# Kernel tuning notes

Measured on AMD Instinct MI355X. Metric: run time of the kernel, lower is better.

The kernel has to match this reference:

```python
import jax, jax.numpy as jnp
import numpy as np
import math

B, N, F = 16, 1024, 1024
OUT = 1024

def setup_inputs() -> dict:
    key = jax.random.key(0)
    k1, k2, k3, k4 = jax.random.split(key, 4)
    prott5_emd = jax.random.normal(k1, (B, N, F), dtype=jnp.float32)
    # shared (dense) normalized adjacency, as the original applies one adj to every sample
    adj = jax.random.uniform(k2, (N, N), dtype=jnp.float32)
    adj = adj / jnp.sum(adj, axis=1, keepdims=True)  # row-normalize like a GCN propagation matrix
    h0 = jax.random.normal(k3, (B, N, F), dtype=jnp.float32)
    stdv = 1.0 / math.sqrt(OUT)
    weight = jax.random.uniform(k4, (F, OUT), minval=-stdv, maxval=stdv, dtype=jnp.float32)
    return {"prott5_emd": prott5_emd, "adj": adj, "h0": h0, "weight": weight,
            "lamda": 0.5, "alpha": 0.1, "l": 1}

def reference(prott5_emd, adj, h0, weight, lamda, alpha, l):
    # GraphConvolution (GCNII-style), variant=False, residual=False
    theta = min(1.0, math.log(lamda / l + 1.0))  # static python scalar
    # batched aggregation: adj @ x_i for every sample i  ->  [B, N, F]
    hi = jnp.einsum('nm,bmf->bnf', adj, prott5_emd)
    support = (1.0 - alpha) * hi + alpha * h0          # affine combine with initial features
    out = theta * jnp.einsum('bnf,fo->bno', support, weight) + (1.0 - theta) * support
    return out
```

## Files before the change

### kernel.cpp

```cpp
#include <hip/hip_runtime.h>
#include <hip/hip_bf16.h>

typedef __attribute__((ext_vector_type(8))) short bf16x8;
typedef __attribute__((ext_vector_type(4))) float f32x4;
typedef __attribute__((ext_vector_type(4))) unsigned int u32x4;
typedef __attribute__((ext_vector_type(2))) unsigned int u32x2;

__device__ __forceinline__ float b2f(unsigned short u) {
  unsigned int x = ((unsigned int)u) << 16;
  float f;
  __builtin_memcpy(&f, &x, 4);
  return f;
}
__device__ __forceinline__ unsigned short f2b(float f) {
  __hip_bfloat16 h = __float2bfloat16(f);
  unsigned short u;
  __builtin_memcpy(&u, &h, 2);
  return u;
}

__global__ __launch_bounds__(256) void conv_transpose64(
    const float* __restrict__ src, unsigned short* __restrict__ dst,
    int R, int C) {
  __shared__ unsigned short tile[64][68];
  const int b = blockIdx.z;
  const float* s = src + (size_t)b * R * C;
  unsigned short* d = dst + (size_t)b * R * C;
  const int r0 = blockIdx.y * 64, c0 = blockIdx.x * 64;
  const int t = threadIdx.x;
#pragma unroll
  for (int p = 0; p < 4; ++p) {
    const int id = t + 256 * p;
    const int r = id >> 4, c4 = (id & 15) * 4;
    f32x4 v = *(const f32x4*)(s + (size_t)(r0 + r) * C + (c0 + c4));
#pragma unroll
    for (int j = 0; j < 4; ++j) tile[r][c4 + j] = f2b(v[j]);
  }
  __syncthreads();
#pragma unroll
  for (int p = 0; p < 2; ++p) {
    const int id = t + 256 * p;
    const int oc = id >> 3, cr8 = (id & 7) * 8;
    u32x4 v;
    unsigned short* pv = (unsigned short*)&v;
#pragma unroll
    for (int j = 0; j < 8; ++j) pv[j] = tile[cr8 + j][oc];
    *(u32x4*)(d + (size_t)(c0 + oc) * R + (r0 + cr8)) = v;
  }
}

__global__ __launch_bounds__(256) void conv_transpose_wprime(
    const float* __restrict__ src, unsigned short* __restrict__ dst,
    float scale, float diag) {
  __shared__ float tile[64][65];
  const int r0 = blockIdx.y * 64, c0 = blockIdx.x * 64;
  const int t = threadIdx.x;
#pragma unroll
  for (int p = 0; p < 4; ++p) {
    const int id = t + 256 * p;
    const int r = id >> 4, c4 = (id & 15) * 4;
    f32x4 v = *(const f32x4*)(src + (size_t)(r0 + r) * 1024 + (c0 + c4));
#pragma unroll
    for (int j = 0; j < 4; ++j) tile[r][c4 + j] = v[j];
  }
  __syncthreads();
#pragma unroll
  for (int p = 0; p < 2; ++p) {
    const int id = t + 256 * p;
    const int oc = id >> 3, cr8 = (id & 7) * 8;
    u32x4 v;
    unsigned short* pv = (unsigned short*)&v;
#pragma unroll
    for (int j = 0; j < 8; ++j) {
      const int o = c0 + oc, f = r0 + cr8 + j;
      float val = scale * tile[cr8 + j][oc] + (o == f ? diag : 0.f);
      pv[j] = f2b(val);
    }
    *(u32x4*)(dst + (size_t)(c0 + oc) * 1024 + (r0 + cr8)) = v;
  }
}

__global__ __launch_bounds__(256) void conv_bf16(const float* __restrict__ src,
                                                 unsigned short* __restrict__ dst,
                                                 int n) {
  const int i = (blockIdx.x * 256 + threadIdx.x) * 4;
  if (i >= n) return;
  f32x4 v = *(const f32x4*)(src + i);
  unsigned short o[4];
#pragma unroll
  for (int j = 0; j < 4; ++j) o[j] = f2b(v[j]);
  u32x2 pk;
  __builtin_memcpy(&pk, o, 8);
  *(u32x2*)(dst + i) = pk;
}

__global__ __launch_bounds__(256) void fuse_h0(
    const unsigned short* __restrict__ Sp, const float* __restrict__ Hp,
    unsigned short* __restrict__ So) {
  const size_t i = ((size_t)blockIdx.x * 256 + threadIdx.x) * 8;
  const u32x4 sv = *(const u32x4*)(Sp + i);
  const f32x4 ha = *(const f32x4*)(Hp + i);
  const f32x4 hb = *(const f32x4*)(Hp + i + 4);
  u32x4 ov;
#pragma unroll
  for (int w = 0; w < 4; ++w) {
    const float hlo = (w < 2) ? ha[2 * w] : hb[2 * w - 4];
    const float hhi = (w < 2) ? ha[2 * w + 1] : hb[2 * w - 3];
    const float r0 = b2f((unsigned short)(sv[w] & 0xffffu)) + 0.1f * hlo;
    const float r1 = b2f((unsigned short)(sv[w] >> 16)) + 0.1f * hhi;
    ov[w] = (unsigned int)f2b(r0) | ((unsigned int)f2b(r1) << 16);
  }
  *(u32x4*)(So + i) = ov;
}

__device__ __forceinline__ void stage_tile16(unsigned short* ldsbase,
                                             const unsigned short* __restrict__ gbase,
                                             size_t rowbase, int half, int k0,
                                             int t, int wv) {
#pragma unroll
  for (int l = 0; l < 2; ++l) {
    const int id = l * 512 + t;
    const int rl = id >> 3, c = id & 7;
    const int gc = (c ^ (rl & 7)) << 3;
    const unsigned short* g = gbase + (rowbase + half * 128 + rl) * 1024 + k0 + gc;
    unsigned short* dst = ldsbase + half * 8192 + (l * 512 + wv * 64) * 8;
    __builtin_amdgcn_global_load_lds(
        (const __attribute__((address_space(1))) unsigned int*)g,
        (__attribute__((address_space(3))) unsigned int*)dst, 16, 0, 0);
  }
}

#define LOAD_A(MH)                                                     \
  {                                                                    \
    const unsigned short* Ard = lds[rd * 2 + 0];                       \
    _Pragma("unroll") for (int mi = 0; mi < 4; ++mi)                   \
        _Pragma("unroll") for (int kk = 0; kk < 2; ++kk) {             \
      const int row = wm + (MH)*64 + mi * 16 + (lane & 15);            \
      const int ch = ((kk * 4 + (lane >> 4)) ^ (row & 7)) << 3;        \
      areg[mi][kk] = *(const bf16x8*)(Ard + row * 64 + ch);            \
    }                                                                  \
  }
#define LOAD_B(NH, BR)                                                 \
  {                                                                    \
    const unsigned short* Brd = lds[rd * 2 + 1];                       \
    _Pragma("unroll") for (int nj = 0; nj < 2; ++nj)                   \
        _Pragma("unroll") for (int kk = 0; kk < 2; ++kk) {             \
      const int row = wn + (NH)*32 + nj * 16 + (lane & 15);            \
      const int ch = ((kk * 4 + (lane >> 4)) ^ (row & 7)) << 3;        \
      BR[nj][kk] = *(const bf16x8*)(Brd + row * 64 + ch);              \
    }                                                                  \
  }
#define MFMA_Q(MH, NH, BR)                                             \
  do {                                                                 \
    __builtin_amdgcn_s_setprio(1);                                     \
    _Pragma("unroll") for (int mi = 0; mi < 4; ++mi)                   \
        _Pragma("unroll") for (int nj = 0; nj < 2; ++nj)               \
            _Pragma("unroll") for (int kk = 0; kk < 2; ++kk)           \
        acc[(MH)*4 + mi][(NH)*2 + nj] =                                \
        __builtin_amdgcn_mfma_f32_16x16x32_bf16(                       \
            areg[mi][kk], BR[nj][kk], acc[(MH)*4 + mi][(NH)*2 + nj],   \
            0, 0, 0);                                                  \
    __builtin_amdgcn_s_setprio(0);                                     \
  } while (0)
#define LGKM0                                          \
  asm volatile("s_waitcnt lgkmcnt(0)" ::: "memory");   \
  __builtin_amdgcn_sched_barrier(0)
#define BAR __builtin_amdgcn_s_barrier()

__global__ __launch_bounds__(512, 2) void gemm1(
    const unsigned short* __restrict__ A, const unsigned short* __restrict__ BT,
    unsigned short* __restrict__ Cq, float c0) {
  constexpr int NT = 16;
  constexpr size_t NF = 1024ull * 1024ull;
  __shared__ unsigned short lds[4][16384];
  const int bid = blockIdx.x;
  const int nid = (bid & 7) * 32 + (bid >> 3);
  const size_t m0 = (size_t)(nid >> 6) * 256, n0 = (size_t)(nid & 63) * 256;
  const int t = threadIdx.x, lane = t & 63, wv = t >> 6;
  const int wm = (wv >> 2) * 128, wn = (wv & 3) * 64;

  f32x4 acc[8][4];
#pragma unroll
  for (int i = 0; i < 8; ++i)
#pragma unroll
    for (int j = 0; j < 4; ++j) acc[i][j] = (f32x4){0.f, 0.f, 0.f, 0.f};
  bf16x8 areg[4][2], b0r[2][2], b1r[2][2];

  stage_tile16(lds[0], A, m0, 0, 0, t, wv);
  stage_tile16(lds[0], A, m0, 1, 0, t, wv);
  stage_tile16(lds[1], BT, n0, 0, 0, t, wv);
  stage_tile16(lds[1], BT, n0, 1, 0, t, wv);
  stage_tile16(lds[3], BT, n0, 0, 64, t, wv);
  stage_tile16(lds[2], A, m0, 0, 64, t, wv);
  asm volatile("s_waitcnt vmcnt(4)" ::: "memory");
  BAR;

  for (int tt = 0; tt < NT; ++tt) {
    const int rd = tt & 1, wr = rd ^ 1;
    LOAD_A(0);
    LOAD_B(0, b0r);
    if (tt + 1 < NT) stage_tile16(lds[wr * 2 + 1], BT, n0, 1, (tt + 1) * 64, t, wv);
    BAR; LGKM0; MFMA_Q(0, 0, b0r); BAR;
    LOAD_B(1, b1r);
    if (tt + 1 < NT) stage_tile16(lds[wr * 2 + 0], A, m0, 1, (tt + 1) * 64, t, wv);
    BAR; LGKM0; MFMA_Q(0, 1, b1r); BAR;
    LOAD_A(1);
    if (tt + 2 < NT) stage_tile16(lds[rd * 2 + 1], BT, n0, 0, (tt + 2) * 64, t, wv);
    BAR; LGKM0; MFMA_Q(1, 1, b1r); BAR;
    if (tt + 2 < NT) stage_tile16(lds[rd * 2 + 0], A, m0, 0, (tt + 2) * 64, t, wv);
    BAR; LGKM0; MFMA_Q(1, 0, b0r);
    asm volatile("s_waitcnt vmcnt(4)" ::: "memory");
    BAR;
  }

  const size_t base = (n0 >> 10) * NF + (n0 & 1023) + m0 * 1024;
  unsigned short* Cb = Cq + base;
#pragma unroll
  for (int mi = 0; mi < 8; ++mi) {
#pragma unroll
    for (int r = 0; r < 4; ++r) {
      const int lrow = wm + mi * 16 + (lane >> 4) * 4 + r;
#pragma unroll
      for (int nj = 0; nj < 4; ++nj) {
        const int lcol = wn + nj * 16 + (lane & 15);
        Cb[(size_t)lrow * 1024 + lcol] = f2b(c0 * acc[mi][nj][r]);
      }
    }
  }
}

__global__ __launch_bounds__(512, 2) void gemm2(
    const unsigned short* __restrict__ A, const unsigned short* __restrict__ BT,
    float* __restrict__ Co) {
  constexpr int NT = 16;
  __shared__ unsigned short lds[4][16384];
  const int bid = blockIdx.x;
  const int nid = (bid & 7) * 32 + (bid >> 3);
  const size_t m0 = (size_t)(nid >> 2) * 256, n0 = (size_t)(nid & 3) * 256;
  const int t = threadIdx.x, lane = t & 63, wv = t >> 6;
  const int wm = (wv >> 2) * 128, wn = (wv & 3) * 64;

  f32x4 acc[8][4];
#pragma unroll
  for (int i = 0; i < 8; ++i)
#pragma unroll
    for (int j = 0; j < 4; ++j) acc[i][j] = (f32x4){0.f, 0.f, 0.f, 0.f};
  bf16x8 areg[4][2], b0r[2][2], b1r[2][2];

  stage_tile16(lds[0], A, m0, 0, 0, t, wv);
  stage_tile16(lds[0], A, m0, 1, 0, t, wv);
  stage_tile16(lds[1], BT, n0, 0, 0, t, wv);
  stage_tile16(lds[1], BT, n0, 1, 0, t, wv);
  stage_tile16(lds[3], BT, n0, 0, 64, t, wv);
  stage_tile16(lds[2], A, m0, 0, 64, t, wv);
  asm volatile("s_waitcnt vmcnt(4)" ::: "memory");
  BAR;

  for (int tt = 0; tt < NT; ++tt) {
    const int rd = tt & 1, wr = rd ^ 1;
    LOAD_A(0);
    LOAD_B(0, b0r);
    if (tt + 1 < NT) stage_tile16(lds[wr * 2 + 1], BT, n0, 1, (tt + 1) * 64, t, wv);
    BAR; LGKM0; MFMA_Q(0, 0, b0r); BAR;
    LOAD_B(1, b1r);
    if (tt + 1 < NT) stage_tile16(lds[wr * 2 + 0], A, m0, 1, (tt + 1) * 64, t, wv);
    BAR; LGKM0; MFMA_Q(0, 1, b1r); BAR;
    LOAD_A(1);
    if (tt + 2 < NT) stage_tile16(lds[rd * 2 + 1], BT, n0, 0, (tt + 2) * 64, t, wv);
    BAR; LGKM0; MFMA_Q(1, 1, b1r); BAR;
    if (tt + 2 < NT) stage_tile16(lds[rd * 2 + 0], A, m0, 0, (tt + 2) * 64, t, wv);
    BAR; LGKM0; MFMA_Q(1, 0, b0r);
    asm volatile("s_waitcnt vmcnt(4)" ::: "memory");
    BAR;
  }

  float* Cb = Co + m0 * 1024 + n0;
#pragma unroll
  for (int mi = 0; mi < 8; ++mi) {
#pragma unroll
    for (int r = 0; r < 4; ++r) {
      const int lrow = wm + mi * 16 + (lane >> 4) * 4 + r;
#pragma unroll
      for (int nj = 0; nj < 4; ++nj) {
        const int lcol = wn + nj * 16 + (lane & 15);
        Cb[(size_t)lrow * 1024 + lcol] = acc[mi][nj][r];
      }
    }
  }
}

#undef LOAD_A
#undef LOAD_B
#undef MFMA_Q
#undef LGKM0
#undef BAR

extern "C" void kernel_launch(void* const* d_in, const int* in_sizes, int n_in,
                              void* d_out, int out_size, void* d_ws,
                              size_t ws_size, hipStream_t stream) {
  const float* X = (const float*)d_in[0];
  const float* adj = (const float*)d_in[1];
  const float* h0 = (const float*)d_in[2];
  const float* W = (const float*)d_in[3];
  float* out = (float*)d_out;

  const size_t NF = 1024ull * 1024ull;
  unsigned short* XT = (unsigned short*)d_ws;
  unsigned short* WT = XT + 16 * NF;
  unsigned short* AJ = WT + NF;
  unsigned short* SP = AJ + NF;

  const float theta = 0.405465108f;

  conv_transpose64<<<dim3(16, 16, 16), 256, 0, stream>>>(X, XT, 1024, 1024);
  conv_transpose_wprime<<<dim3(16, 16, 1), 256, 0, stream>>>(
      W, WT, theta, 1.0f - theta);
  conv_bf16<<<dim3(1024), 256, 0, stream>>>(adj, AJ, 1024 * 1024);

  gemm1<<<dim3(256), 512, 0, stream>>>(AJ, XT, SP, 0.9f);
  fuse_h0<<<dim3(8192), 256, 0, stream>>>(SP, h0, XT);
  gemm2<<<dim3(256), 512, 0, stream>>>(XT, WT, out);
}
```

Before: 120.0 us.

## Fuse h0 residual combine into gemm2 A-tile staging through registers

Drops the separate fuse_h0 kernel. gemm2 now loads the bf16 support tile and fp32 h0 directly into registers, combines them, converts to bf16 and writes the swizzled result into LDS. This removes one launch and a full write and re-read of the intermediate tensor. In exchange, A tiles go through registers instead of async global_load_lds, which raises register pressure, and the pipeline schedule of waits and barriers is reworked, which may expose load latency.

```diff
diff --git a/kernel.cpp b/kernel.cpp
--- a/kernel.cpp
+++ b/kernel.cpp
@@ -92,25 +92,6 @@
   u32x2 pk;
   __builtin_memcpy(&pk, o, 8);
   *(u32x2*)(dst + i) = pk;
-}
-
-__global__ __launch_bounds__(256) void fuse_h0(
-    const unsigned short* __restrict__ Sp, const float* __restrict__ Hp,
-    unsigned short* __restrict__ So) {
-  const size_t i = ((size_t)blockIdx.x * 256 + threadIdx.x) * 8;
-  const u32x4 sv = *(const u32x4*)(Sp + i);
-  const f32x4 ha = *(const f32x4*)(Hp + i);
-  const f32x4 hb = *(const f32x4*)(Hp + i + 4);
-  u32x4 ov;
-#pragma unroll
-  for (int w = 0; w < 4; ++w) {
-    const float hlo = (w < 2) ? ha[2 * w] : hb[2 * w - 4];
-    const float hhi = (w < 2) ? ha[2 * w + 1] : hb[2 * w - 3];
-    const float r0 = b2f((unsigned short)(sv[w] & 0xffffu)) + 0.1f * hlo;
-    const float r1 = b2f((unsigned short)(sv[w] >> 16)) + 0.1f * hhi;
-    ov[w] = (unsigned int)f2b(r0) | ((unsigned int)f2b(r1) << 16);
-  }
-  *(u32x4*)(So + i) = ov;
 }
 
 __device__ __forceinline__ void stage_tile16(unsigned short* ldsbase,
@@ -229,9 +210,37 @@
   }
 }
 
+#define G2_LOADSRC(H, K0, SV, HA, HB)                                        \
+  {                                                                          \
+    _Pragma("unroll") for (int l = 0; l < 2; ++l) {                          \
+      const int id = l * 512 + t, rl = id >> 3, cc = id & 7;                 \
+      const size_t grow = m0 + (H)*128 + rl;                                 \
+      SV[l] = *(const u32x4*)(Sp + grow * 1024 + (K0) + cc * 8);             \
+      HA[l] = *(const f32x4*)(Hp + grow * 1024 + (K0) + cc * 8);             \
+      HB[l] = *(const f32x4*)(Hp + grow * 1024 + (K0) + cc * 8 + 4);         \
+    }                                                                        \
+  }
+#define G2_CVTWRITE(H, WB, SV, HA, HB)                                       \
+  {                                                                          \
+    _Pragma("unroll") for (int l = 0; l < 2; ++l) {                          \
+      const int id = l * 512 + t, rl = id >> 3, cc = id & 7;                 \
+      u32x4 ov;                                                              \
+      _Pragma("unroll") for (int w = 0; w < 4; ++w) {                        \
+        const float hlo = (w < 2) ? HA[l][2 * w] : HB[l][2 * w - 4];         \
+        const float hhi = (w < 2) ? HA[l][2 * w + 1] : HB[l][2 * w - 3];     \
+        const float r0 =                                                     \
+            b2f((unsigned short)(SV[l][w] & 0xffffu)) + 0.1f * hlo;          \
+        const float r1 = b2f((unsigned short)(SV[l][w] >> 16)) + 0.1f * hhi; \
+        ov[w] = (unsigned int)f2b(r0) | ((unsigned int)f2b(r1) << 16);       \
+      }                                                                      \
+      *(u32x4*)(&lds[(WB)*2 + 0][(H)*8192 + rl * 64 +                        \
+                                 ((cc ^ (rl & 7)) << 3)]) = ov;              \
+    }                                                                        \
+  }
+
 __global__ __launch_bounds__(512, 2) void gemm2(
-    const unsigned short* __restrict__ A, const unsigned short* __restrict__ BT,
-    float* __restrict__ Co) {
+    const unsigned short* __restrict__ Sp, const unsigned short* __restrict__ BT,
+    const float* __restrict__ Hp, float* __restrict__ Co) {
   constexpr int NT = 16;
   __shared__ unsigned short lds[4][16384];
   const int bid = blockIdx.x;
@@ -246,31 +255,43 @@
 #pragma unroll
     for (int j = 0; j < 4; ++j) acc[i][j] = (f32x4){0.f, 0.f, 0.f, 0.f};
   bf16x8 areg[4][2], b0r[2][2], b1r[2][2];
-
-  stage_tile16(lds[0], A, m0, 0, 0, t, wv);
-  stage_tile16(lds[0], A, m0, 1, 0, t, wv);
+  u32x4 sv0[2], sv1[2];
+  f32x4 ha0[2], hb0[2], ha1[2], hb1[2];
+
+  G2_LOADSRC(0, 0, sv0, ha0, hb0);
+  G2_CVTWRITE(0, 0, sv0, ha0, hb0);
+  G2_LOADSRC(1, 0, sv1, ha1, hb1);
+  G2_CVTWRITE(1, 0, sv1, ha1, hb1);
   stage_tile16(lds[1], BT, n0, 0, 0, t, wv);
   stage_tile16(lds[1], BT, n0, 1, 0, t, wv);
   stage_tile16(lds[3], BT, n0, 0, 64, t, wv);
-  stage_tile16(lds[2], A, m0, 0, 64, t, wv);
-  asm volatile("s_waitcnt vmcnt(4)" ::: "memory");
+  asm volatile("s_waitcnt vmcnt(2)" ::: "memory");
+  LGKM0;
   BAR;
 
   for (int tt = 0; tt < NT; ++tt) {
     const int rd = tt & 1, wr = rd ^ 1;
+    const int k1 = (tt + 1) * 64;
+    const bool hasA = (tt + 1 < NT);
     LOAD_A(0);
     LOAD_B(0, b0r);
-    if (tt + 1 < NT) stage_tile16(lds[wr * 2 + 1], BT, n0, 1, (tt + 1) * 64, t, wv);
+    if (hasA) {
+      stage_tile16(lds[wr * 2 + 1], BT, n0, 1, k1, t, wv);
+      G2_LOADSRC(0, k1, sv0, ha0, hb0);
+    }
     BAR; LGKM0; MFMA_Q(0, 0, b0r); BAR;
     LOAD_B(1, b1r);
-    if (tt + 1 < NT) stage_tile16(lds[wr * 2 + 0], A, m0, 1, (tt + 1) * 64, t, wv);
+    if (hasA) {
+      G2_CVTWRITE(0, wr, sv0, ha0, hb0);
+      G2_LOADSRC(1, k1, sv1, ha1, hb1);
+    }
     BAR; LGKM0; MFMA_Q(0, 1, b1r); BAR;
     LOAD_A(1);
+    if (hasA) G2_CVTWRITE(1, wr, sv1, ha1, hb1);
     if (tt + 2 < NT) stage_tile16(lds[rd * 2 + 1], BT, n0, 0, (tt + 2) * 64, t, wv);
     BAR; LGKM0; MFMA_Q(1, 1, b1r); BAR;
-    if (tt + 2 < NT) stage_tile16(lds[rd * 2 + 0], A, m0, 0, (tt + 2) * 64, t, wv);
-    BAR; LGKM0; MFMA_Q(1, 0, b0r);
-    asm volatile("s_waitcnt vmcnt(4)" ::: "memory");
+    MFMA_Q(1, 0, b0r);
+    asm volatile("s_waitcnt vmcnt(2)" ::: "memory");
     BAR;
   }
 
@@ -294,6 +315,8 @@
 #undef MFMA_Q
 #undef LGKM0
 #undef BAR
+#undef G2_LOADSRC
+#undef G2_CVTWRITE
 
 extern "C" void kernel_launch(void* const* d_in, const int* in_sizes, int n_in,
                               void* d_out, int out_size, void* d_ws,
@@ -318,6 +341,5 @@
   conv_bf16<<<dim3(1024), 256, 0, stream>>>(adj, AJ, 1024 * 1024);
 
   gemm1<<<dim3(256), 512, 0, stream>>>(AJ, XT, SP, 0.9f);
-  fuse_h0<<<dim3(8192), 256, 0, stream>>>(SP, h0, XT);
-  gemm2<<<dim3(256), 512, 0, stream>>>(XT, WT, out);
-}
+  gemm2<<<dim3(256), 512, 0, stream>>>(SP, WT, h0, out);
+}
```

New measurement: 139.8 us. 16.5% more time.

## Fuse h0 combine into gemm1 epilogue and merge prep kernels into one launch

Applied to the files above, without the earlier changes.

The separate fuse_h0 pass is removed. The gemm1 epilogue now reads h0 in fp32 directly and writes 0.9*acc + 0.1*h0 as bf16, which avoids one round trip of the intermediate support tensor through memory. The three preprocessing kernels (X transpose, W' transpose, adj conversion) become one launch, selected by blockIdx.z. The cost is that gemm1's epilogue now does scalar, less coalesced fp32 loads of h0, and the prep launch has divergent block roles.

```diff
diff --git a/kernel.cpp b/kernel.cpp
--- a/kernel.cpp
+++ b/kernel.cpp
@@ -19,20 +19,67 @@
   return u;
 }
 
-__global__ __launch_bounds__(256) void conv_transpose64(
-    const float* __restrict__ src, unsigned short* __restrict__ dst,
-    int R, int C) {
+__global__ __launch_bounds__(256) void prep_all(
+    const float* __restrict__ X, const float* __restrict__ adj,
+    const float* __restrict__ W, unsigned short* __restrict__ XT,
+    unsigned short* __restrict__ AJ, unsigned short* __restrict__ WT,
+    float theta) {
+  const int z = blockIdx.z;
+  const int t = threadIdx.x;
+  const int r0 = blockIdx.y * 64, c0 = blockIdx.x * 64;
+
+  if (z == 17) {
+#pragma unroll
+    for (int p = 0; p < 4; ++p) {
+      const int id = t + 256 * p;
+      const int r = id >> 4, c4 = (id & 15) * 4;
+      f32x4 v = *(const f32x4*)(adj + (size_t)(r0 + r) * 1024 + (c0 + c4));
+      unsigned short o[4];
+#pragma unroll
+      for (int j = 0; j < 4; ++j) o[j] = f2b(v[j]);
+      u32x2 pk;
+      __builtin_memcpy(&pk, o, 8);
+      *(u32x2*)(AJ + (size_t)(r0 + r) * 1024 + (c0 + c4)) = pk;
+    }
+    return;
+  }
+
+  if (z == 16) {
+    __shared__ float tile[64][65];
+#pragma unroll
+    for (int p = 0; p < 4; ++p) {
+      const int id = t + 256 * p;
+      const int r = id >> 4, c4 = (id & 15) * 4;
+      f32x4 v = *(const f32x4*)(W + (size_t)(r0 + r) * 1024 + (c0 + c4));
+#pragma unroll
+      for (int j = 0; j < 4; ++j) tile[r][c4 + j] = v[j];
+    }
+    __syncthreads();
+#pragma unroll
+    for (int p = 0; p < 2; ++p) {
+      const int id = t + 256 * p;
+      const int oc = id >> 3, cr8 = (id & 7) * 8;
+      u32x4 v;
+      unsigned short* pv = (unsigned short*)&v;
+#pragma unroll
+      for (int j = 0; j < 8; ++j) {
+        const int o = c0 + oc, f = r0 + cr8 + j;
+        float val = theta * tile[cr8 + j][oc] + (o == f ? (1.0f - theta) : 0.f);
+        pv[j] = f2b(val);
+      }
+      *(u32x4*)(WT + (size_t)(c0 + oc) * 1024 + (r0 + cr8)) = v;
+    }
+    return;
+  }
+
   __shared__ unsigned short tile[64][68];
-  const int b = blockIdx.z;
-  const float* s = src + (size_t)b * R * C;
-  unsigned short* d = dst + (size_t)b * R * C;
-  const int r0 = blockIdx.y * 64, c0 = blockIdx.x * 64;
-  const int t = threadIdx.x;
+  const float* s = X + (size_t)z * 1024 * 1024;
+  unsigned short* d = XT + (size_t)z * 1024 * 1024;
 #pragma unroll
   for (int p = 0; p < 4; ++p) {
     const int id = t + 256 * p;
     const int r = id >> 4, c4 = (id & 15) * 4;
-    f32x4 v = *(const f32x4*)(s + (size_t)(r0 + r) * C + (c0 + c4));
+    f32x4 v = *(const f32x4*)(s + (size_t)(r0 + r) * 1024 + (c0 + c4));
 #pragma unroll
     for (int j = 0; j < 4; ++j) tile[r][c4 + j] = f2b(v[j]);
   }
@@ -45,72 +92,8 @@
     unsigned short* pv = (unsigned short*)&v;
 #pragma unroll
     for (int j = 0; j < 8; ++j) pv[j] = tile[cr8 + j][oc];
-    *(u32x4*)(d + (size_t)(c0 + oc) * R + (r0 + cr8)) = v;
-  }
-}
-
-__global__ __launch_bounds__(256) void conv_transpose_wprime(
-    const float* __restrict__ src, unsigned short* __restrict__ dst,
-    float scale, float diag) {
-  __shared__ float tile[64][65];
-  const int r0 = blockIdx.y * 64, c0 = blockIdx.x * 64;
-  const int t = threadIdx.x;
-#pragma unroll
-  for (int p = 0; p < 4; ++p) {
-    const int id = t + 256 * p;
-    const int r = id >> 4, c4 = (id & 15) * 4;
-    f32x4 v = *(const f32x4*)(src + (size_t)(r0 + r) * 1024 + (c0 + c4));
-#pragma unroll
-    for (int j = 0; j < 4; ++j) tile[r][c4 + j] = v[j];
-  }
-  __syncthreads();
-#pragma unroll
-  for (int p = 0; p < 2; ++p) {
-    const int id = t + 256 * p;
-    const int oc = id >> 3, cr8 = (id & 7) * 8;
-    u32x4 v;
-    unsigned short* pv = (unsigned short*)&v;
-#pragma unroll
-    for (int j = 0; j < 8; ++j) {
-      const int o = c0 + oc, f = r0 + cr8 + j;
-      float val = scale * tile[cr8 + j][oc] + (o == f ? diag : 0.f);
-      pv[j] = f2b(val);
-    }
-    *(u32x4*)(dst + (size_t)(c0 + oc) * 1024 + (r0 + cr8)) = v;
-  }
-}
-
-__global__ __launch_bounds__(256) void conv_bf16(const float* __restrict__ src,
-                                                 unsigned short* __restrict__ dst,
-                                                 int n) {
-  const int i = (blockIdx.x * 256 + threadIdx.x) * 4;
-  if (i >= n) return;
-  f32x4 v = *(const f32x4*)(src + i);
-  unsigned short o[4];
-#pragma unroll
-  for (int j = 0; j < 4; ++j) o[j] = f2b(v[j]);
-  u32x2 pk;
-  __builtin_memcpy(&pk, o, 8);
-  *(u32x2*)(dst + i) = pk;
-}
-
-__global__ __launch_bounds__(256) void fuse_h0(
-    const unsigned short* __restrict__ Sp, const float* __restrict__ Hp,
-    unsigned short* __restrict__ So) {
-  const size_t i = ((size_t)blockIdx.x * 256 + threadIdx.x) * 8;
-  const u32x4 sv = *(const u32x4*)(Sp + i);
-  const f32x4 ha = *(const f32x4*)(Hp + i);
-  const f32x4 hb = *(const f32x4*)(Hp + i + 4);
-  u32x4 ov;
-#pragma unroll
-  for (int w = 0; w < 4; ++w) {
-    const float hlo = (w < 2) ? ha[2 * w] : hb[2 * w - 4];
-    const float hhi = (w < 2) ? ha[2 * w + 1] : hb[2 * w - 3];
-    const float r0 = b2f((unsigned short)(sv[w] & 0xffffu)) + 0.1f * hlo;
-    const float r1 = b2f((unsigned short)(sv[w] >> 16)) + 0.1f * hhi;
-    ov[w] = (unsigned int)f2b(r0) | ((unsigned int)f2b(r1) << 16);
-  }
-  *(u32x4*)(So + i) = ov;
+    *(u32x4*)(d + (size_t)(c0 + oc) * 1024 + (r0 + cr8)) = v;
+  }
 }
 
 __device__ __forceinline__ void stage_tile16(unsigned short* ldsbase,
@@ -167,9 +150,43 @@
   __builtin_amdgcn_sched_barrier(0)
 #define BAR __builtin_amdgcn_s_barrier()
 
+#define GEMM_KLOOP                                                            \
+  for (int tt = 0; tt < NT; ++tt) {                                           \
+    const int rd = tt & 1, wr = rd ^ 1;                                       \
+    LOAD_A(0);                                                                \
+    LOAD_B(0, b0r);                                                           \
+    if (tt + 1 < NT)                                                          \
+      stage_tile16(lds[wr * 2 + 1], BT, n0, 1, (tt + 1) * 64, t, wv);         \
+    BAR; LGKM0; MFMA_Q(0, 0, b0r); BAR;                                       \
+    LOAD_B(1, b1r);                                                           \
+    if (tt + 1 < NT)                                                          \
+      stage_tile16(lds[wr * 2 + 0], A, m0, 1, (tt + 1) * 64, t, wv);          \
+    BAR; LGKM0; MFMA_Q(0, 1, b1r); BAR;                                       \
+    LOAD_A(1);                                                                \
+    if (tt + 2 < NT)                                                          \
+      stage_tile16(lds[rd * 2 + 1], BT, n0, 0, (tt + 2) * 64, t, wv);         \
+    BAR; LGKM0; MFMA_Q(1, 1, b1r); BAR;                                       \
+    if (tt + 2 < NT)                                                          \
+      stage_tile16(lds[rd * 2 + 0], A, m0, 0, (tt + 2) * 64, t, wv);          \
+    BAR; LGKM0; MFMA_Q(1, 0, b0r);                                            \
+    asm volatile("s_waitcnt vmcnt(4)" ::: "memory");                          \
+    BAR;                                                                      \
+  }
+
+#define GEMM_PROLOGUE                                                         \
+  stage_tile16(lds[0], A, m0, 0, 0, t, wv);                                   \
+  stage_tile16(lds[0], A, m0, 1, 0, t, wv);                                   \
+  stage_tile16(lds[1], BT, n0, 0, 0, t, wv);                                  \
+  stage_tile16(lds[1], BT, n0, 1, 0, t, wv);                                  \
+  stage_tile16(lds[3], BT, n0, 0, 64, t, wv);                                 \
+  stage_tile16(lds[2], A, m0, 0, 64, t, wv);                                  \
+  asm volatile("s_waitcnt vmcnt(4)" ::: "memory");                            \
+  BAR;
+
 __global__ __launch_bounds__(512, 2) void gemm1(
     const unsigned short* __restrict__ A, const unsigned short* __restrict__ BT,
-    unsigned short* __restrict__ Cq, float c0) {
+    const float* __restrict__ E, unsigned short* __restrict__ Cq,
+    float c0, float c1) {
   constexpr int NT = 16;
   constexpr size_t NF = 1024ull * 1024ull;
   __shared__ unsigned short lds[4][16384];
@@ -186,34 +203,11 @@
     for (int j = 0; j < 4; ++j) acc[i][j] = (f32x4){0.f, 0.f, 0.f, 0.f};
   bf16x8 areg[4][2], b0r[2][2], b1r[2][2];
 
-  stage_tile16(lds[0], A, m0, 0, 0, t, wv);
-  stage_tile16(lds[0], A, m0, 1, 0, t, wv);
-  stage_tile16(lds[1], BT, n0, 0, 0, t, wv);
-  stage_tile16(lds[1], BT, n0, 1, 0, t, wv);
-  stage_tile16(lds[3], BT, n0, 0, 64, t, wv);
-  stage_tile16(lds[2], A, m0, 0, 64, t, wv);
-  asm volatile("s_waitcnt vmcnt(4)" ::: "memory");
-  BAR;
-
-  for (int tt = 0; tt < NT; ++tt) {
-    const int rd = tt & 1, wr = rd ^ 1;
-    LOAD_A(0);
-    LOAD_B(0, b0r);
-    if (tt + 1 < NT) stage_tile16(lds[wr * 2 + 1], BT, n0, 1, (tt + 1) * 64, t, wv);
-    BAR; LGKM0; MFMA_Q(0, 0, b0r); BAR;
-    LOAD_B(1, b1r);
-    if (tt + 1 < NT) stage_tile16(lds[wr * 2 + 0], A, m0, 1, (tt + 1) * 64, t, wv);
-    BAR; LGKM0; MFMA_Q(0, 1, b1r); BAR;
-    LOAD_A(1);
-    if (tt + 2 < NT) stage_tile16(lds[rd * 2 + 1], BT, n0, 0, (tt + 2) * 64, t, wv);
-    BAR; LGKM0; MFMA_Q(1, 1, b1r); BAR;
-    if (tt + 2 < NT) stage_tile16(lds[rd * 2 + 0], A, m0, 0, (tt + 2) * 64, t, wv);
-    BAR; LGKM0; MFMA_Q(1, 0, b0r);
-    asm volatile("s_waitcnt vmcnt(4)" ::: "memory");
-    BAR;
-  }
+  GEMM_PROLOGUE
+  GEMM_KLOOP
 
   const size_t base = (n0 >> 10) * NF + (n0 & 1023) + m0 * 1024;
+  const float* Eb = E + base;
   unsigned short* Cb = Cq + base;
 #pragma unroll
   for (int mi = 0; mi < 8; ++mi) {
@@ -223,7 +217,9 @@
 #pragma unroll
       for (int nj = 0; nj < 4; ++nj) {
         const int lcol = wn + nj * 16 + (lane & 15);
-        Cb[(size_t)lrow * 1024 + lcol] = f2b(c0 * acc[mi][nj][r]);
+        const float v =
+            c0 * acc[mi][nj][r] + c1 * Eb[(size_t)lrow * 1024 + lcol];
+        Cb[(size_t)lrow * 1024 + lcol] = f2b(v);
       }
     }
   }
@@ -247,32 +243,8 @@
     for (int j = 0; j < 4; ++j) acc[i][j] = (f32x4){0.f, 0.f, 0.f, 0.f};
   bf16x8 areg[4][2], b0r[2][2], b1r[2][2];
 
-  stage_tile16(lds[0], A, m0, 0, 0, t, wv);
-  stage_tile16(lds[0], A, m0, 1, 0, t, wv);
-  stage_tile16(lds[1], BT, n0, 0, 0, t, wv);
-  stage_tile16(lds[1], BT, n0, 1, 0, t, wv);
-  stage_tile16(lds[3], BT, n0, 0, 64, t, wv);
-  stage_tile16(lds[2], A, m0, 0, 64, t, wv);
-  asm volatile("s_waitcnt vmcnt(4)" ::: "memory");
-  BAR;
-
-  for (int tt = 0; tt < NT; ++tt) {
-    const int rd = tt & 1, wr = rd ^ 1;
-    LOAD_A(0);
-    LOAD_B(0, b0r);
-    if (tt + 1 < NT) stage_tile16(lds[wr * 2 + 1], BT, n0, 1, (tt + 1) * 64, t, wv);
-    BAR; LGKM0; MFMA_Q(0, 0, b0r); BAR;
-    LOAD_B(1, b1r);
-    if (tt + 1 < NT) stage_tile16(lds[wr * 2 + 0], A, m0, 1, (tt + 1) * 64, t, wv);
-    BAR; LGKM0; MFMA_Q(0, 1, b1r); BAR;
-    LOAD_A(1);
-    if (tt + 2 < NT) stage_tile16(lds[rd * 2 + 1], BT, n0, 0, (tt + 2) * 64, t, wv);
-    BAR; LGKM0; MFMA_Q(1, 1, b1r); BAR;
-    if (tt + 2 < NT) stage_tile16(lds[rd * 2 + 0], A, m0, 0, (tt + 2) * 64, t, wv);
-    BAR; LGKM0; MFMA_Q(1, 0, b0r);
-    asm volatile("s_waitcnt vmcnt(4)" ::: "memory");
-    BAR;
-  }
+  GEMM_PROLOGUE
+  GEMM_KLOOP
 
   float* Cb = Co + m0 * 1024 + n0;
 #pragma unroll
@@ -294,6 +266,8 @@
 #undef MFMA_Q
 #undef LGKM0
 #undef BAR
+#undef GEMM_KLOOP
+#undef GEMM_PROLOGUE
 
 extern "C" void kernel_launch(void* const* d_in, const int* in_sizes, int n_in,
                               void* d_out, int out_size, void* d_ws,
@@ -308,16 +282,12 @@
   unsigned short* XT = (unsigned short*)d_ws;
   unsigned short* WT = XT + 16 * NF;
   unsigned short* AJ = WT + NF;
-  unsigned short* SP = AJ + NF;
+  unsigned short* S = AJ + NF;
 
   const float theta = 0.405465108f;
 
-  conv_transpose64<<<dim3(16, 16, 16), 256, 0, stream>>>(X, XT, 1024, 1024);
-  conv_transpose_wprime<<<dim3(16, 16, 1), 256, 0, stream>>>(
-      W, WT, theta, 1.0f - theta);
-  conv_bf16<<<dim3(1024), 256, 0, stream>>>(adj, AJ, 1024 * 1024);
-
-  gemm1<<<dim3(256), 512, 0, stream>>>(AJ, XT, SP, 0.9f);
-  fuse_h0<<<dim3(8192), 256, 0, stream>>>(SP, h0, XT);
-  gemm2<<<dim3(256), 512, 0, stream>>>(XT, WT, out);
-}
+  prep_all<<<dim3(16, 16, 18), 256, 0, stream>>>(X, adj, W, XT, AJ, WT, theta);
+
+  gemm1<<<dim3(256), 512, 0, stream>>>(AJ, XT, h0, S, 0.9f, 0.1f);
+  gemm2<<<dim3(256), 512, 0, stream>>>(S, WT, out);
+}
```

After: 111.5 us. -7.0%, faster.
